# Kernel tuning notes

Measured on AMD Instinct MI355X. Metric: run time of the kernel, lower is better.

## Reference

```python
import jax, jax.numpy as jnp
import numpy as np

B, L, D = 4, 2048, 1024
DI = D            # d_inner = expand * d_model, expand=1
N = 8             # d_state
K = 4             # d_conv
R = 64            # dt_rank = ceil(d_model/16)
EPS = 1e-5


def setup_inputs() -> dict:
    key = jax.random.key(0)
    ks = jax.random.split(key, 10)
    hidden_states = jax.random.normal(ks[0], (B, L, D), dtype=jnp.float32)
    norm_w = jnp.ones((D,), dtype=jnp.float32)
    in_proj_w = jax.random.normal(ks[1], (2 * DI, D), dtype=jnp.float32) * 0.02
    conv_w = jax.random.normal(ks[2], (DI, 1, K), dtype=jnp.float32) * 0.2
    conv_b = jnp.zeros((DI,), dtype=jnp.float32)
    x_proj_w = jax.random.normal(ks[3], (R + 2 * N, DI), dtype=jnp.float32) * 0.02
    dt_proj_w = jax.random.normal(ks[4], (DI, R), dtype=jnp.float32) * 0.1
    # bias init so softplus(bias) lands in a sane dt range (~e^-4 .. e^-1)
    dt_proj_b = jax.random.uniform(ks[5], (DI,), minval=-4.0, maxval=-1.0, dtype=jnp.float32)
    # S4D-real style init: A = -[1..N] per channel
    A_log = jnp.log(jnp.broadcast_to(jnp.arange(1, N + 1, dtype=jnp.float32), (DI, N)))
    D_skip = jnp.ones((DI,), dtype=jnp.float32)
    out_proj_w = jax.random.normal(ks[6], (D, DI), dtype=jnp.float32) * 0.02
    return {
        "hidden_states": hidden_states, "norm_w": norm_w,
        "in_proj_w": in_proj_w, "conv_w": conv_w, "conv_b": conv_b,
        "x_proj_w": x_proj_w, "dt_proj_w": dt_proj_w, "dt_proj_b": dt_proj_b,
        "A_log": A_log, "D_skip": D_skip, "out_proj_w": out_proj_w,
    }


def _rmsnorm(x, w):
    return x * jax.lax.rsqrt(jnp.mean(x * x, axis=-1, keepdims=True) + EPS) * w


def _mamba_block(hidden_states, norm_w, in_proj_w, conv_w, conv_b,
                 x_proj_w, dt_proj_w, dt_proj_b, A_log, D_skip, out_proj_w):
    x = _rmsnorm(hidden_states, norm_w)                      # [B,L,D]
    xz = jnp.einsum('bld,ed->ble', x, in_proj_w)             # [B,L,2*DI]
    x, z = jnp.split(xz, 2, axis=-1)                         # [B,L,DI] each
    # causal depthwise conv1d (torch pads d_conv-1 both sides then slices :L => left pad only)
    xc = jnp.transpose(x, (0, 2, 1))                         # [B,DI,L]
    k = conv_w.shape[-1]
    xc = jax.lax.conv_general_dilated(
        xc, conv_w, window_strides=(1,), padding=[(k - 1, 0)],
        dimension_numbers=('NCH', 'OIH', 'NCH'), feature_group_count=DI)
    x = jax.nn.silu(jnp.transpose(xc, (0, 2, 1)) + conv_b)   # [B,L,DI]
    # input-dependent dt, B, C
    dbl = jnp.einsum('bld,ed->ble', x, x_proj_w)             # [B,L,R+2N]
    dt, Bm, Cm = jnp.split(dbl, [R, R + N], axis=-1)
    dt = jax.nn.softplus(jnp.einsum('blr,dr->bld', dt, dt_proj_w) + dt_proj_b)  # [B,L,DI]
    A = -jnp.exp(A_log)                                      # [DI,N]
    dA = jnp.exp(dt[..., None] * A)                          # [B,L,DI,N]
    dBx = dt[..., None] * Bm[:, :, None, :] * x[..., None]   # [B,L,DI,N]

    def step(h, inp):
        a_t, bx_t, c_t = inp                                 # [B,DI,N],[B,DI,N],[B,N]
        h = a_t * h + bx_t
        y = jnp.einsum('bdn,bn->bd', h, c_t)
        return h, y

    h0 = jnp.zeros((hidden_states.shape[0], DI, N), dtype=x.dtype)
    _, ys = jax.lax.scan(step, h0, (jnp.transpose(dA, (1, 0, 2, 3)),
                                    jnp.transpose(dBx, (1, 0, 2, 3)),
                                    jnp.transpose(Cm, (1, 0, 2))))
    y = jnp.transpose(ys, (1, 0, 2)) + D_skip * x            # [B,L,DI]
    y = y * jax.nn.silu(z)
    out = jnp.einsum('bld,ed->ble', y, out_proj_w)           # [B,L,D]
    return out  # use_res=False


def reference(hidden_states, norm_w, in_proj_w, conv_w, conv_b,
              x_proj_w, dt_proj_w, dt_proj_b, A_log, D_skip, out_proj_w):
    return _mamba_block(hidden_states, norm_w, in_proj_w, conv_w, conv_b,
                        x_proj_w, dt_proj_w, dt_proj_b, A_log, D_skip, out_proj_w)
```

## Files before the change

### kernel.cpp

```cpp
#include <hip/hip_runtime.h>
#include <stdint.h>
#include <stddef.h>


typedef unsigned short u16;
typedef unsigned int u32;
typedef _Float16 f16;
typedef __attribute__((ext_vector_type(8))) _Float16 half8;
typedef __attribute__((ext_vector_type(4))) _Float16 half4;
typedef __attribute__((ext_vector_type(4))) float f32x4;

#define LSEQ 2048
#define DMODEL 1024
#define NSTATE 8
#define NCHUNK 64
#define CHUNKL 32
#define NROWS 8192
#define WS_NEED (115ull << 20)

__device__ __forceinline__ void gload_lds16(const void* g, void* l) {
    __builtin_amdgcn_global_load_lds((__attribute__((address_space(1))) void*)g,
                                     (__attribute__((address_space(3))) void*)l,
                                     16, 0, 0);
}

__global__ __launch_bounds__(256) void sentinel_kernel(float* __restrict__ out, int n) {
    int i = blockIdx.x * 256 + threadIdx.x;
    if (i < n) out[i] = 999.0f;
}

#define T0 524288
#define T1 20480
#define T2 16384
#define T3 262144
#define WCVT_BLK 3216
#define ZERO_BLK 640
__global__ __launch_bounds__(256) void prep_kernel(const float* __restrict__ s0,
                                                   const float* __restrict__ s1,
                                                   const float* __restrict__ s2,
                                                   const float* __restrict__ s3,
                                                   f16* __restrict__ d0, f16* __restrict__ d1,
                                                   f16* __restrict__ d2, f16* __restrict__ d3,
                                                   float* __restrict__ dblz,
                                                   const float* __restrict__ X,
                                                   const float* __restrict__ W,
                                                   f16* __restrict__ O) {
    const int bx = blockIdx.x;
    const int tid = threadIdx.x;
    if (bx < WCVT_BLK) {
        int idx = bx * 256 + tid;
        const float* s; f16* d; int i;
        if (idx < T0) { s = s0; d = d0; i = idx; }
        else if (idx < T0 + T1) { s = s1; d = d1; i = idx - T0; }
        else if (idx < T0 + T1 + T2) { s = s2; d = d2; i = idx - T0 - T1; }
        else { s = s3; d = d3; i = idx - T0 - T1 - T2; }
        f32x4 v = *(const f32x4*)(s + (size_t)i * 4);
        half4 o; o[0] = (f16)v[0]; o[1] = (f16)v[1]; o[2] = (f16)v[2]; o[3] = (f16)v[3];
        *(half4*)(d + (size_t)i * 4) = o;
    } else if (bx < WCVT_BLK + ZERO_BLK) {
        int i = (bx - WCVT_BLK) * 256 + tid;
        const f32x4 z4 = {0.f, 0.f, 0.f, 0.f};
        ((f32x4*)dblz)[i] = z4;
    } else {
        const int row = bx - (WCVT_BLK + ZERO_BLK);
        f32x4 u = *(const f32x4*)(X + (size_t)row * DMODEL + tid * 4);
        float ss = u[0]*u[0] + u[1]*u[1] + u[2]*u[2] + u[3]*u[3];
        for (int off = 32; off; off >>= 1) ss += __shfl_down(ss, off, 64);
        __shared__ float red[4];
        if ((tid & 63) == 0) red[tid >> 6] = ss;
        __syncthreads();
        float tot = red[0] + red[1] + red[2] + red[3];
        float scale = rsqrtf(tot * (1.0f / DMODEL) + 1e-5f);
        f32x4 w = *(const f32x4*)(W + tid * 4);
        half4 o;
        o[0] = (f16)(u[0] * scale * w[0]); o[1] = (f16)(u[1] * scale * w[1]);
        o[2] = (f16)(u[2] * scale * w[2]); o[3] = (f16)(u[3] * scale * w[3]);
        *(half4*)(O + (size_t)row * DMODEL + tid * 4) = o;
    }
}


#define G4 asm volatile("s_waitcnt vmcnt(4)" ::: "memory")
#define G2 asm volatile("s_waitcnt vmcnt(2)" ::: "memory")
#define G0 asm volatile("s_waitcnt vmcnt(0)" ::: "memory")
#define GN (void)0

#define SA8(tt, hf) do { \
    gload_lds16(aG + (size_t)(tt) * 64 + (size_t)(hf) * hA, \
                sA + (((tt) & 1) * 16384) + (hf) * 8192 + ldsW); \
    gload_lds16(aG + (size_t)(tt) * 64 + (size_t)(hf) * hA + rA, \
                sA + (((tt) & 1) * 16384) + (hf) * 8192 + 4096 + ldsW); \
} while (0)
#define SB8(tt, hf) do { \
    gload_lds16(bG + (size_t)(tt) * 64 + (size_t)(hf) * hB, \
                sB + (((tt) & 1) * 16384) + (hf) * 8192 + ldsW); \
    gload_lds16(bG + (size_t)(tt) * 64 + (size_t)(hf) * hB + rB, \
                sB + (((tt) & 1) * 16384) + (hf) * 8192 + 4096 + ldsW); \
} while (0)

#define PHASE(MH, NH, STAGE_STMT, GUARD_STMT) do { \
    half8 paf[4][2], pbf[2][2]; \
    _Pragma("unroll") \
    for (int f_ = 0; f_ < 4; f_++) { \
        paf[f_][0] = *(const half8*)(sAb + rdA0 + ((MH) * 4 + f_) * 1024); \
        paf[f_][1] = *(const half8*)(sAb + rdA1 + ((MH) * 4 + f_) * 1024); \
    } \
    _Pragma("unroll") \
    for (int g_ = 0; g_ < 2; g_++) { \
        pbf[g_][0] = *(const half8*)(sBb + rdB0 + ((NH) * 2 + g_) * 1024); \
        pbf[g_][1] = *(const half8*)(sBb + rdB1 + ((NH) * 2 + g_) * 1024); \
    } \
    STAGE_STMT; \
    GUARD_STMT; \
    __builtin_amdgcn_s_barrier(); \
    __builtin_amdgcn_sched_barrier(0); \
    __builtin_amdgcn_s_setprio(1); \
    _Pragma("unroll") \
    for (int f_ = 0; f_ < 4; f_++) \
        _Pragma("unroll") \
        for (int g_ = 0; g_ < 2; g_++) { \
            acc[(MH) * 4 + f_][(NH) * 2 + g_] = __builtin_amdgcn_mfma_f32_16x16x32_f16( \
                paf[f_][0], pbf[g_][0], acc[(MH) * 4 + f_][(NH) * 2 + g_], 0, 0, 0); \
            acc[(MH) * 4 + f_][(NH) * 2 + g_] = __builtin_amdgcn_mfma_f32_16x16x32_f16( \
                paf[f_][1], pbf[g_][1], acc[(MH) * 4 + f_][(NH) * 2 + g_], 0, 0, 0); \
        } \
    __builtin_amdgcn_s_setprio(0); \
    __builtin_amdgcn_s_barrier(); \
    __builtin_amdgcn_sched_barrier(0); \
} while (0)

template <int EPI>
__global__ __launch_bounds__(512, 2) void gemm8p(const f16* __restrict__ Ap, int lda,
                                                 const f16* __restrict__ Bm, int ldb,
                                                 void* __restrict__ C0, void* __restrict__ C1,
                                                 int KT) {
    __shared__ alignas(16) f16 sA[2 * 256 * 64];
    __shared__ alignas(16) f16 sB[2 * 256 * 64];
    const int tid = threadIdx.x;
    const int wave = tid >> 6, lane = tid & 63;
    const int wm = wave >> 2, wn = wave & 3;
    const int cl = lane & 15, q = lane >> 4;
    const int tm = blockIdx.x, tn = blockIdx.y;

    const int srow = tid >> 3;
    const int skc = (tid & 7) ^ (srow & 7);
    const f16* aG = Ap + (size_t)(tm * 256 + srow) * lda + skc * 8;
    const f16* bG = Bm + (size_t)(tn * 256 + srow) * ldb + skc * 8;
    const size_t rA = (size_t)64 * lda, hA = (size_t)128 * lda;
    const size_t rB = (size_t)64 * ldb, hB = (size_t)128 * ldb;
    const int ldsW = wave * 512;

    const int swz0 = (q ^ (cl & 7)) << 3;
    const int swz1 = ((4 + q) ^ (cl & 7)) << 3;
    const int rdA0 = (wm * 128 + cl) * 64 + swz0;
    const int rdA1 = (wm * 128 + cl) * 64 + swz1;
    const int rdB0 = (wn * 64 + cl) * 64 + swz0;
    const int rdB1 = (wn * 64 + cl) * 64 + swz1;

    f32x4 acc[8][4];
    const f32x4 zero4 = {0.f, 0.f, 0.f, 0.f};
#pragma unroll
    for (int f = 0; f < 8; f++)
#pragma unroll
        for (int g = 0; g < 4; g++) acc[f][g] = zero4;

    SA8(0, 0); SB8(0, 0); SA8(0, 1); SB8(0, 1);
    G4;
    __builtin_amdgcn_s_barrier();
    __builtin_amdgcn_sched_barrier(0);

    for (int t = 0; t < KT - 1; t++) {
        const f16* sAb = sA + (t & 1) * 16384;
        const f16* sBb = sB + (t & 1) * 16384;
        PHASE(0, 0, SA8(t + 1, 0), G4);
        PHASE(1, 0, SB8(t + 1, 0), G4);
        PHASE(0, 1, SA8(t + 1, 1), GN);
        PHASE(1, 1, SB8(t + 1, 1), G4);
    }
    {
        const int t = KT - 1;
        const f16* sAb = sA + (t & 1) * 16384;
        const f16* sBb = sB + (t & 1) * 16384;
        PHASE(0, 0, GN, G2);
        PHASE(1, 0, GN, G0);
        PHASE(0, 1, GN, GN);
        PHASE(1, 1, GN, GN);
    }

    const int rowb = tm * 256 + wm * 128 + q * 4;
    const int colb = tn * 256 + wn * 64 + cl;
#pragma unroll
    for (int f = 0; f < 8; f++)
#pragma unroll
        for (int r = 0; r < 4; r++) {
            size_t ro = (size_t)(rowb + f * 16 + r) * 1024;
#pragma unroll
            for (int g = 0; g < 4; g++) {
                int gc = colb + g * 16;
                float v = acc[f][g][r];
                if (EPI == 0) {
                    if (gc < 1024) ((f16*)C0)[ro + gc] = (f16)v;
                    else           ((f16*)C1)[ro + gc - 1024] = (f16)v;
                } else {
                    ((float*)C0)[ro + gc] = v;
                }
            }
        }
}

template <int EPI, int AF32>
__global__ __launch_bounds__(256) void gemm_f16(const void* __restrict__ Ap, int lda,
                                                const f16* __restrict__ Bm, int ldb,
                                                void* __restrict__ C0, void* __restrict__ C1,
                                                int ldc, int N, int klen,
                                                const float* __restrict__ fbias) {
    __shared__ alignas(16) f16 sA[128 * 64];
    __shared__ alignas(16) f16 sB[128 * 64];
    const int tid = threadIdx.x;
    const int wave = tid >> 6, lane = tid & 63;
    const int wm = (wave >> 1) * 64, wn = (wave & 1) * 64;
    const int tm = blockIdx.x, tn = blockIdx.y;
    const int q = lane >> 4, cl = lane & 15;
    const int kbeg = blockIdx.z * klen;

    f32x4 acc[4][4];
    const f32x4 zero4 = {0.f, 0.f, 0.f, 0.f};
#pragma unroll
    for (int t = 0; t < 4; t++)
#pragma unroll
        for (int u = 0; u < 4; u++) acc[t][u] = zero4;

    int rS[4], gkS[4];
#pragma unroll
    for (int j = 0; j < 4; j++) {
        int c = wave * 256 + j * 64 + lane;
        rS[j] = c >> 3;
        gkS[j] = (c & 7) ^ (rS[j] & 7);
    }

    for (int k0 = kbeg; k0 < kbeg + klen; k0 += 64) {
        __syncthreads();
#pragma unroll
        for (int j = 0; j < 4; j++) {
            int ldsoff = (wave * 256 + j * 64) * 8;
            if (!AF32) {
                int ga = tm * 128 + rS[j];
                gload_lds16((const f16*)Ap + (size_t)ga * lda + k0 + gkS[j] * 8, sA + ldsoff);
            }
            int gb = tn * 128 + rS[j];
            if (gb >= N) gb = N - 1;
            gload_lds16(Bm + (size_t)gb * ldb + k0 + gkS[j] * 8, sB + ldsoff);
        }
        __syncthreads();

        half8 af[4][2], bf[4][2];
#pragma unroll
        for (int t = 0; t < 4; t++)
#pragma unroll
            for (int s = 0; s < 2; s++) {
                int m = wm + t * 16 + cl;
                int kc = s * 4 + q;
                if (AF32) {
                    const float* pa = (const float*)Ap + (size_t)(tm * 128 + m) * lda + k0 + kc * 8;
                    f32x4 v0 = *(const f32x4*)pa, v1 = *(const f32x4*)(pa + 4);
                    half8 a;
                    a[0] = (f16)v0[0]; a[1] = (f16)v0[1]; a[2] = (f16)v0[2]; a[3] = (f16)v0[3];
                    a[4] = (f16)v1[0]; a[5] = (f16)v1[1]; a[6] = (f16)v1[2]; a[7] = (f16)v1[3];
                    af[t][s] = a;
                } else {
                    af[t][s] = *(const half8*)(sA + m * 64 + ((kc ^ (m & 7)) << 3));
                }
                int n = wn + t * 16 + cl;
                bf[t][s] = *(const half8*)(sB + n * 64 + ((kc ^ (n & 7)) << 3));
            }
#pragma unroll
        for (int t = 0; t < 4; t++)
#pragma unroll
            for (int u = 0; u < 4; u++) {
                acc[t][u] = __builtin_amdgcn_mfma_f32_16x16x32_f16(af[t][0], bf[u][0], acc[t][u], 0, 0, 0);
                acc[t][u] = __builtin_amdgcn_mfma_f32_16x16x32_f16(af[t][1], bf[u][1], acc[t][u], 0, 0, 0);
            }
    }

    const int rowbase = tm * 128 + wm + q * 4;
    const int colbase = tn * 128 + wn + cl;
#pragma unroll
    for (int t = 0; t < 4; t++)
#pragma unroll
        for (int r = 0; r < 4; r++) {
            size_t rb_ = (size_t)(rowbase + t * 16 + r) * ldc;
            size_t rb1 = (size_t)(rowbase + t * 16 + r) * 1024;
#pragma unroll
            for (int u = 0; u < 4; u++) {
                int gcol = colbase + u * 16;
                float v = acc[t][u][r];
                if (EPI == 0) {
                    if (gcol < 1024) ((f16*)C0)[rb1 + gcol] = (f16)v;
                    else             ((f16*)C1)[rb1 + gcol - 1024] = (f16)v;
                } else if (EPI == 1) {
                    if (gcol < N) ((float*)C0)[rb_ + gcol] = v;
                } else if (EPI == 2) {
                    if (gcol < N) atomicAdd((float*)C0 + rb_ + gcol, v);
                } else {
                    if (gcol < N) {
                        float sv = v + fbias[gcol];
                        sv = (sv > 15.f) ? sv : log1pf(__expf(sv));
                        ((f16*)C0)[rb_ + gcol] = (f16)sv;
                    }
                }
            }
        }
}

template __global__ void gemm_f16<3, 1>(const void*, int, const f16*, int,
                                        void*, void*, int, int, int, const float*);
template __global__ void gemm_f16<0, 0>(const void*, int, const f16*, int,
                                        void*, void*, int, int, int, const float*);

__global__ __launch_bounds__(256) void dtproj_kernel(const float* __restrict__ Ap,
                                                     const f16* __restrict__ Wt,
                                                     f16* __restrict__ Cd,
                                                     const float* __restrict__ fbias) {
    __shared__ alignas(16) f16 sW[128 * 64];
    const int tid = threadIdx.x;
    const int wave = tid >> 6, lane = tid & 63;
    const int q = lane >> 4, cl = lane & 15;
    const int tm = blockIdx.x, tn = blockIdx.y;

#pragma unroll
    for (int j = 0; j < 4; j++) {
        int c = wave * 256 + j * 64 + lane;
        int row = c >> 3;
        int kc = (c & 7) ^ (row & 7);
        gload_lds16(Wt + (size_t)(tn * 128 + row) * 64 + kc * 8,
                    sW + (wave * 256 + j * 64) * 8);
    }

    half8 af[2][2];
#pragma unroll
    for (int t = 0; t < 2; t++)
#pragma unroll
        for (int s = 0; s < 2; s++) {
            int m = wave * 32 + t * 16 + cl;
            const float* pa = Ap + (size_t)(tm * 128 + m) * 80 + (s * 4 + q) * 8;
            f32x4 v0 = *(const f32x4*)pa, v1 = *(const f32x4*)(pa + 4);
            half8 a;
            a[0] = (f16)v0[0]; a[1] = (f16)v0[1]; a[2] = (f16)v0[2]; a[3] = (f16)v0[3];
            a[4] = (f16)v1[0]; a[5] = (f16)v1[1]; a[6] = (f16)v1[2]; a[7] = (f16)v1[3];
            af[t][s] = a;
        }

    __syncthreads();

    f32x4 acc[2][8];
    const f32x4 zero4 = {0.f, 0.f, 0.f, 0.f};
#pragma unroll
    for (int t = 0; t < 2; t++)
#pragma unroll
        for (int fn = 0; fn < 8; fn++) acc[t][fn] = zero4;

#pragma unroll
    for (int fn = 0; fn < 8; fn++) {
        int n = fn * 16 + cl;
#pragma unroll
        for (int s = 0; s < 2; s++) {
            half8 bf = *(const half8*)(sW + n * 64 + (((s * 4 + q) ^ (n & 7)) << 3));
            acc[0][fn] = __builtin_amdgcn_mfma_f32_16x16x32_f16(af[0][s], bf, acc[0][fn], 0, 0, 0);
            acc[1][fn] = __builtin_amdgcn_mfma_f32_16x16x32_f16(af[1][s], bf, acc[1][fn], 0, 0, 0);
        }
    }

    const int rowb = tm * 128 + wave * 32 + q * 4;
    const int colb = tn * 128 + cl;
#pragma unroll
    for (int t = 0; t < 2; t++)
#pragma unroll
        for (int r = 0; r < 4; r++) {
            size_t ro = (size_t)(rowb + t * 16 + r) * 1024;
#pragma unroll
            for (int fn = 0; fn < 8; fn++) {
                int gc = colb + fn * 16;
                float sv = acc[t][fn][r] + fbias[gc];
                sv = (sv > 15.f) ? sv : log1pf(__expf(sv));
                Cd[ro + gc] = (f16)sv;
            }
        }
}

__global__ __launch_bounds__(256) void conv_silu_kernel(const f16* __restrict__ x,
                                                        const float* __restrict__ cw,
                                                        const float* __restrict__ cb,
                                                        f16* __restrict__ xc) {
    const int rg = blockIdx.x;
    const int d = blockIdx.y * 256 + threadIdx.x;
    const int row0 = rg * 4;
    const int l0 = row0 & (LSEQ - 1);
    float w0 = cw[d * 4], w1 = cw[d * 4 + 1], w2 = cw[d * 4 + 2], w3 = cw[d * 4 + 3];
    float bias = cb[d];
    float v[7];
#pragma unroll
    for (int j = 0; j < 7; j++) {
        int ll = l0 - 3 + j;
        v[j] = (ll >= 0) ? (float)x[(size_t)(row0 - 3 + j) * 1024 + d] : 0.f;
    }
#pragma unroll
    for (int i = 0; i < 4; i++) {
        float acc = bias + w0 * v[i] + w1 * v[i + 1] + w2 * v[i + 2] + w3 * v[i + 3];
        xc[(size_t)(row0 + i) * 1024 + d] = (f16)(acc / (1.f + __expf(-acc)));
    }
}

__global__ __launch_bounds__(256) void scan1_kernel(const f16* __restrict__ dt,
                                                    const f16* __restrict__ xc,
                                                    const float* __restrict__ dbl,
                                                    const float* __restrict__ A_log,
                                                    float* __restrict__ hF,
                                                    float* __restrict__ Pb) {
    const int d = blockIdx.x * 256 + threadIdx.x;
    const int c = blockIdx.y;
    const int b = blockIdx.z;
    __shared__ float sB[CHUNKL * NSTATE];
    sB[threadIdx.x] = dbl[(size_t)(b * LSEQ + c * CHUNKL + (threadIdx.x >> 3)) * 80 + 64 + (threadIdx.x & 7)];
    __syncthreads();
    f32x4 al0 = *(const f32x4*)(A_log + d * 8);
    f32x4 al1 = *(const f32x4*)(A_log + d * 8 + 4);
    float Aa[NSTATE];
#pragma unroll
    for (int n = 0; n < 4; n++) { Aa[n] = -__expf(al0[n]); Aa[n + 4] = -__expf(al1[n]); }
    float h[NSTATE], P[NSTATE];
#pragma unroll
    for (int n = 0; n < NSTATE; n++) { h[n] = 0.f; P[n] = 1.f; }
    const f16* pdt = dt + (size_t)(b * LSEQ + c * CHUNKL) * 1024 + d;
    const f16* pxc = xc + (size_t)(b * LSEQ + c * CHUNKL) * 1024 + d;
    for (int lb = 0; lb < CHUNKL; lb += 8) {
        float vdt[8], vxc[8];
#pragma unroll
        for (int j = 0; j < 8; j++) {
            vdt[j] = (float)pdt[(size_t)(lb + j) * 1024];
            vxc[j] = (float)pxc[(size_t)(lb + j) * 1024];
        }
#pragma unroll
        for (int j = 0; j < 8; j++) {
            float dtx = vdt[j] * vxc[j];
#pragma unroll
            for (int n = 0; n < NSTATE; n++) {
                float e = __expf(Aa[n] * vdt[j]);
                h[n] = e * h[n] + dtx * sB[(lb + j) * 8 + n];
                P[n] *= e;
            }
        }
    }
    size_t base = ((size_t)(c * 4 + b) * 1024 + d) * 8;
    f32x4 o;
    o[0]=h[0]; o[1]=h[1]; o[2]=h[2]; o[3]=h[3]; *(f32x4*)(hF + base) = o;
    o[0]=h[4]; o[1]=h[5]; o[2]=h[6]; o[3]=h[7]; *(f32x4*)(hF + base + 4) = o;
    o[0]=P[0]; o[1]=P[1]; o[2]=P[2]; o[3]=P[3]; *(f32x4*)(Pb + base) = o;
    o[0]=P[4]; o[1]=P[5]; o[2]=P[6]; o[3]=P[7]; *(f32x4*)(Pb + base + 4) = o;
}

__global__ __launch_bounds__(256) void combine_kernel(const float* __restrict__ hF,
                                                      const float* __restrict__ Pb,
                                                      float* __restrict__ h0) {
    int t = blockIdx.x * 256 + threadIdx.x;
    int n = t & 7, dd = (t >> 3) & 1023, b = t >> 13;
    size_t off = (size_t)(b * 1024 + dd) * 8 + n;
    float h = 0.f;
#pragma unroll 8
    for (int c = 0; c < NCHUNK; c++) {
        size_t idx = (size_t)c * 32768 + off;
        h0[idx] = h;
        h = fmaf(Pb[idx], h, hF[idx]);
    }
}

__global__ __launch_bounds__(256) void scan2_kernel(const f16* __restrict__ dt,
                                                    const f16* __restrict__ xc,
                                                    const float* __restrict__ dbl,
                                                    const float* __restrict__ A_log,
                                                    const float* __restrict__ h0,
                                                    const f16* __restrict__ z,
                                                    const float* __restrict__ Dsk,
                                                    f16* __restrict__ yout) {
    const int d = blockIdx.x * 256 + threadIdx.x;
    const int c = blockIdx.y;
    const int b = blockIdx.z;
    __shared__ float sB[CHUNKL * NSTATE];
    __shared__ float sC[CHUNKL * NSTATE];
    {
        size_t rb = (size_t)(b * LSEQ + c * CHUNKL + (threadIdx.x >> 3)) * 80;
        sB[threadIdx.x] = dbl[rb + 64 + (threadIdx.x & 7)];
        sC[threadIdx.x] = dbl[rb + 72 + (threadIdx.x & 7)];
    }
    __syncthreads();
    f32x4 al0 = *(const f32x4*)(A_log + d * 8);
    f32x4 al1 = *(const f32x4*)(A_log + d * 8 + 4);
    float Aa[NSTATE];
#pragma unroll
    for (int n = 0; n < 4; n++) { Aa[n] = -__expf(al0[n]); Aa[n + 4] = -__expf(al1[n]); }
    float h[NSTATE];
    {
        size_t base = ((size_t)(c * 4 + b) * 1024 + d) * 8;
        f32x4 h0a = *(const f32x4*)(h0 + base);
        f32x4 h0b = *(const f32x4*)(h0 + base + 4);
#pragma unroll
        for (int n = 0; n < 4; n++) { h[n] = h0a[n]; h[n + 4] = h0b[n]; }
    }
    const float dval = Dsk[d];
    const size_t rowoff = (size_t)(b * LSEQ + c * CHUNKL) * 1024 + d;
    const f16* pdt = dt + rowoff;
    const f16* pxc = xc + rowoff;
    const f16* pz  = z  + rowoff;
    f16* py = yout + rowoff;
    for (int lb = 0; lb < CHUNKL; lb += 8) {
        float vdt[8], vxc[8], vz[8];
#pragma unroll
        for (int j = 0; j < 8; j++) {
            vdt[j] = (float)pdt[(size_t)(lb + j) * 1024];
            vxc[j] = (float)pxc[(size_t)(lb + j) * 1024];
            vz[j]  = (float)pz[(size_t)(lb + j) * 1024];
        }
#pragma unroll
        for (int j = 0; j < 8; j++) {
            float dtx = vdt[j] * vxc[j];
            float y = 0.f;
#pragma unroll
            for (int n = 0; n < NSTATE; n++) {
                float e = __expf(Aa[n] * vdt[j]);
                h[n] = e * h[n] + dtx * sB[(lb + j) * 8 + n];
                y += h[n] * sC[(lb + j) * 8 + n];
            }
            y += dval * vxc[j];
            y *= vz[j] / (1.f + __expf(-vz[j]));
            py[(size_t)(lb + j) * 1024] = (f16)y;
        }
    }
}

extern "C" void kernel_launch(void* const* d_in, const int* in_sizes, int n_in,
                              void* d_out, int out_size, void* d_ws, size_t ws_size,
                              hipStream_t stream) {
    (void)in_sizes; (void)n_in;
    const float* hidden    = (const float*)d_in[0];
    const float* norm_w    = (const float*)d_in[1];
    const float* in_proj_w = (const float*)d_in[2];
    const float* conv_w    = (const float*)d_in[3];
    const float* conv_b    = (const float*)d_in[4];
    const float* x_proj_w  = (const float*)d_in[5];
    const float* dt_proj_w = (const float*)d_in[6];
    const float* dt_proj_b = (const float*)d_in[7];
    const float* A_log     = (const float*)d_in[8];
    const float* D_skip    = (const float*)d_in[9];
    const float* out_proj_w= (const float*)d_in[10];
    float* out = (float*)d_out;

    if (ws_size < WS_NEED) {
        sentinel_kernel<<<dim3((out_size + 255) / 256), 256, 0, stream>>>(out, out_size);
        return;
    }

    char* ws = (char*)d_ws;
    f16*   xn_h  = (f16*)(ws);
    f16*   xbuf_h= (f16*)(ws + (16ull << 20));
    f16*   zbuf_h= (f16*)(ws + (32ull << 20));
    f16*   xc_h  = (f16*)(ws + (48ull << 20));
    f16*   wih   = (f16*)(ws + (64ull << 20));
    f16*   woh   = (f16*)(ws + (68ull << 20));
    f16*   wxh   = (f16*)(ws + (70ull << 20));
    f16*   wdh   = (f16*)(ws + (70ull << 20) + (512ull << 10));
    float* dbl_f = (float*)(ws + (71ull << 20));
    f16*   dth   = (f16*)(ws + (75ull << 20));
    float* hF    = (float*)(ws + (91ull << 20));
    float* Pb    = (float*)(ws + (99ull << 20));
    float* h0    = (float*)(ws + (107ull << 20));
    f16*   y_h   = xn_h;

    prep_kernel<<<dim3(WCVT_BLK + ZERO_BLK + NROWS), 256, 0, stream>>>(
        in_proj_w, x_proj_w, dt_proj_w, out_proj_w, wih, wxh, wdh, woh,
        dbl_f, hidden, norm_w, xn_h);
    gemm8p<0><<<dim3(32, 8), 512, 0, stream>>>(xn_h, 1024, wih, 1024,
                                               xbuf_h, zbuf_h, 16);
    conv_silu_kernel<<<dim3(NROWS / 4, 4), 256, 0, stream>>>(xbuf_h, conv_w, conv_b, xc_h);
    gemm_f16<2, 0><<<dim3(64, 1, 4), 256, 0, stream>>>(xc_h, 1024, wxh, 1024,
                                                       dbl_f, nullptr, 80, 80, 256, nullptr);
    dtproj_kernel<<<dim3(64, 8), 256, 0, stream>>>(dbl_f, wdh, dth, dt_proj_b);
    scan1_kernel<<<dim3(4, NCHUNK, 4), 256, 0, stream>>>(dth, xc_h, dbl_f, A_log, hF, Pb);
    combine_kernel<<<dim3(128), 256, 0, stream>>>(hF, Pb, h0);
    scan2_kernel<<<dim3(4, NCHUNK, 4), 256, 0, stream>>>(dth, xc_h, dbl_f, A_log, h0,
                                                         zbuf_h, D_skip, y_h);
    gemm_f16<1, 0><<<dim3(64, 8), 256, 0, stream>>>(y_h, 1024, woh, 1024,
                                                    out, nullptr, 1024, 1024, 1024, nullptr);
}
```

Measured before the change: 292.7 us.

## Replace 8-phase ping-pong GEMM schedule with one-barrier-per-tile double buffering

Rewrites the in_proj GEMM main loop so each K-tile issues every global-to-LDS prefetch for the next tile up front, then runs all four MFMA quadrants in one block, reusing A/B fragments across quadrants. A single waitcnt and barrier then closes each tile, replacing the previous eight barriers per tile and the staged vmcnt guards. The aim is to cut barrier and synchronisation overhead and to reuse register fragments. The trade-off is coarser overlap: the loads must fully drain before the next tile, and the setprio interleaving across waves is lost.

Result: faster. 283.7 us (median of 3 runs) (-3.1%).

```diff
diff --git a/kernel.cpp b/kernel.cpp
--- a/kernel.cpp
+++ b/kernel.cpp
@@ -80,11 +80,6 @@
 }
 
 
-#define G4 asm volatile("s_waitcnt vmcnt(4)" ::: "memory")
-#define G2 asm volatile("s_waitcnt vmcnt(2)" ::: "memory")
-#define G0 asm volatile("s_waitcnt vmcnt(0)" ::: "memory")
-#define GN (void)0
-
 #define SA8(tt, hf) do { \
     gload_lds16(aG + (size_t)(tt) * 64 + (size_t)(hf) * hA, \
                 sA + (((tt) & 1) * 16384) + (hf) * 8192 + ldsW); \
@@ -98,39 +93,8 @@
                 sB + (((tt) & 1) * 16384) + (hf) * 8192 + 4096 + ldsW); \
 } while (0)
 
-#define PHASE(MH, NH, STAGE_STMT, GUARD_STMT) do { \
-    half8 paf[4][2], pbf[2][2]; \
-    _Pragma("unroll") \
-    for (int f_ = 0; f_ < 4; f_++) { \
-        paf[f_][0] = *(const half8*)(sAb + rdA0 + ((MH) * 4 + f_) * 1024); \
-        paf[f_][1] = *(const half8*)(sAb + rdA1 + ((MH) * 4 + f_) * 1024); \
-    } \
-    _Pragma("unroll") \
-    for (int g_ = 0; g_ < 2; g_++) { \
-        pbf[g_][0] = *(const half8*)(sBb + rdB0 + ((NH) * 2 + g_) * 1024); \
-        pbf[g_][1] = *(const half8*)(sBb + rdB1 + ((NH) * 2 + g_) * 1024); \
-    } \
-    STAGE_STMT; \
-    GUARD_STMT; \
-    __builtin_amdgcn_s_barrier(); \
-    __builtin_amdgcn_sched_barrier(0); \
-    __builtin_amdgcn_s_setprio(1); \
-    _Pragma("unroll") \
-    for (int f_ = 0; f_ < 4; f_++) \
-        _Pragma("unroll") \
-        for (int g_ = 0; g_ < 2; g_++) { \
-            acc[(MH) * 4 + f_][(NH) * 2 + g_] = __builtin_amdgcn_mfma_f32_16x16x32_f16( \
-                paf[f_][0], pbf[g_][0], acc[(MH) * 4 + f_][(NH) * 2 + g_], 0, 0, 0); \
-            acc[(MH) * 4 + f_][(NH) * 2 + g_] = __builtin_amdgcn_mfma_f32_16x16x32_f16( \
-                paf[f_][1], pbf[g_][1], acc[(MH) * 4 + f_][(NH) * 2 + g_], 0, 0, 0); \
-        } \
-    __builtin_amdgcn_s_setprio(0); \
-    __builtin_amdgcn_s_barrier(); \
-    __builtin_amdgcn_sched_barrier(0); \
-} while (0)
-
 template <int EPI>
-__global__ __launch_bounds__(512, 2) void gemm8p(const f16* __restrict__ Ap, int lda,
+__global__ __launch_bounds__(512, 2) void gemm1b(const f16* __restrict__ Ap, int lda,
                                                  const f16* __restrict__ Bm, int ldb,
                                                  void* __restrict__ C0, void* __restrict__ C1,
                                                  int KT) {
@@ -164,27 +128,75 @@
 #pragma unroll
         for (int g = 0; g < 4; g++) acc[f][g] = zero4;
 
-    SA8(0, 0); SB8(0, 0); SA8(0, 1); SB8(0, 1);
-    G4;
+    SA8(0, 0); SA8(0, 1); SB8(0, 0); SB8(0, 1);
+    asm volatile("s_waitcnt vmcnt(0)" ::: "memory");
     __builtin_amdgcn_s_barrier();
     __builtin_amdgcn_sched_barrier(0);
 
-    for (int t = 0; t < KT - 1; t++) {
+    for (int t = 0; t < KT; t++) {
         const f16* sAb = sA + (t & 1) * 16384;
         const f16* sBb = sB + (t & 1) * 16384;
-        PHASE(0, 0, SA8(t + 1, 0), G4);
-        PHASE(1, 0, SB8(t + 1, 0), G4);
-        PHASE(0, 1, SA8(t + 1, 1), GN);
-        PHASE(1, 1, SB8(t + 1, 1), G4);
-    }
-    {
-        const int t = KT - 1;
-        const f16* sAb = sA + (t & 1) * 16384;
-        const f16* sBb = sB + (t & 1) * 16384;
-        PHASE(0, 0, GN, G2);
-        PHASE(1, 0, GN, G0);
-        PHASE(0, 1, GN, GN);
-        PHASE(1, 1, GN, GN);
+
+        if (t + 1 < KT) { SA8(t + 1, 0); SA8(t + 1, 1); SB8(t + 1, 0); SB8(t + 1, 1); }
+        __builtin_amdgcn_sched_barrier(0);
+
+        half8 a0[4][2], a1[4][2], b0[2][2], b1[2][2];
+#pragma unroll
+        for (int f = 0; f < 4; f++) {
+            a0[f][0] = *(const half8*)(sAb + rdA0 + f * 1024);
+            a0[f][1] = *(const half8*)(sAb + rdA1 + f * 1024);
+        }
+#pragma unroll
+        for (int g = 0; g < 2; g++) {
+            b0[g][0] = *(const half8*)(sBb + rdB0 + g * 1024);
+            b0[g][1] = *(const half8*)(sBb + rdB1 + g * 1024);
+        }
+        __builtin_amdgcn_s_setprio(1);
+#pragma unroll
+        for (int f = 0; f < 4; f++)
+#pragma unroll
+            for (int g = 0; g < 2; g++) {
+                acc[f][g] = __builtin_amdgcn_mfma_f32_16x16x32_f16(a0[f][0], b0[g][0], acc[f][g], 0, 0, 0);
+                acc[f][g] = __builtin_amdgcn_mfma_f32_16x16x32_f16(a0[f][1], b0[g][1], acc[f][g], 0, 0, 0);
+            }
+#pragma unroll
+        for (int g = 0; g < 2; g++) {
+            b1[g][0] = *(const half8*)(sBb + rdB0 + (2 + g) * 1024);
+            b1[g][1] = *(const half8*)(sBb + rdB1 + (2 + g) * 1024);
+        }
+#pragma unroll
+        for (int f = 0; f < 4; f++)
+#pragma unroll
+            for (int g = 0; g < 2; g++) {
+                acc[f][2 + g] = __builtin_amdgcn_mfma_f32_16x16x32_f16(a0[f][0], b1[g][0], acc[f][2 + g], 0, 0, 0);
+                acc[f][2 + g] = __builtin_amdgcn_mfma_f32_16x16x32_f16(a0[f][1], b1[g][1], acc[f][2 + g], 0, 0, 0);
+            }
+#pragma unroll
+        for (int f = 0; f < 4; f++) {
+            a1[f][0] = *(const half8*)(sAb + rdA0 + (4 + f) * 1024);
+            a1[f][1] = *(const half8*)(sAb + rdA1 + (4 + f) * 1024);
+        }
+#pragma unroll
+        for (int f = 0; f < 4; f++)
+#pragma unroll
+            for (int g = 0; g < 2; g++) {
+                acc[4 + f][2 + g] = __builtin_amdgcn_mfma_f32_16x16x32_f16(a1[f][0], b1[g][0], acc[4 + f][2 + g], 0, 0, 0);
+                acc[4 + f][2 + g] = __builtin_amdgcn_mfma_f32_16x16x32_f16(a1[f][1], b1[g][1], acc[4 + f][2 + g], 0, 0, 0);
+            }
+#pragma unroll
+        for (int f = 0; f < 4; f++)
+#pragma unroll
+            for (int g = 0; g < 2; g++) {
+                acc[4 + f][g] = __builtin_amdgcn_mfma_f32_16x16x32_f16(a1[f][0], b0[g][0], acc[4 + f][g], 0, 0, 0);
+                acc[4 + f][g] = __builtin_amdgcn_mfma_f32_16x16x32_f16(a1[f][1], b0[g][1], acc[4 + f][g], 0, 0, 0);
+            }
+        __builtin_amdgcn_s_setprio(0);
+
+        if (t + 1 < KT) {
+            asm volatile("s_waitcnt vmcnt(0)" ::: "memory");
+            __builtin_amdgcn_s_barrier();
+            __builtin_amdgcn_sched_barrier(0);
+        }
     }
 
     const int rowb = tm * 256 + wm * 128 + q * 4;
@@ -577,7 +589,7 @@
     prep_kernel<<<dim3(WCVT_BLK + ZERO_BLK + NROWS), 256, 0, stream>>>(
         in_proj_w, x_proj_w, dt_proj_w, out_proj_w, wih, wxh, wdh, woh,
         dbl_f, hidden, norm_w, xn_h);
-    gemm8p<0><<<dim3(32, 8), 512, 0, stream>>>(xn_h, 1024, wih, 1024,
+    gemm1b<0><<<dim3(32, 8), 512, 0, stream>>>(xn_h, 1024, wih, 1024,
                                                xbuf_h, zbuf_h, 16);
     conv_silu_kernel<<<dim3(NROWS / 4, 4), 256, 0, stream>>>(xbuf_h, conv_w, conv_b, xc_h);
     gemm_f16<2, 0><<<dim3(64, 1, 4), 256, 0, stream>>>(xc_h, 1024, wxh, 1024,
```
